# Kernel tuning notes

Hardware: AMD Instinct MI355X
Metric: run time of the kernel (lower is better)

Reference implementation:

```python
import jax, jax.numpy as jnp
import numpy as np

N_NODES = 50000
N_EDGES = 800000
N_GRAPHS = 512
IN_C, HID, OUT_C = 128, 256, 16


def _mlp(h, w1, b1, w2, b2):
    # PyG-style 2-layer MLP: Linear -> ReLU -> Linear (plain last layer)
    return jax.nn.relu(h @ w1 + b1) @ w2 + b2


def setup_inputs() -> dict:
    key = jax.random.key(0)
    ks = jax.random.split(key, 16)
    x = jax.random.normal(ks[0], (N_NODES, IN_C), dtype=jnp.float32)
    edge_index = jax.random.randint(ks[1], (2, N_EDGES), 0, N_NODES, dtype=jnp.int64)
    batch = jnp.sort(jax.random.randint(ks[2], (N_NODES,), 0, N_GRAPHS, dtype=jnp.int64))

    def lin(k, fan_in, fan_out):
        s = 1.0 / np.sqrt(fan_in)
        return jax.random.uniform(k, (fan_in, fan_out), jnp.float32, -s, s)

    inp = {"x": x, "edge_index": edge_index, "batch": batch}
    dims = [(IN_C, HID), (HID, HID), (HID, HID)]
    ki = 3
    for li, (din, dh) in enumerate(dims):
        inp[f"c{li}_w1"] = lin(ks[ki], din, dh); ki += 1
        inp[f"c{li}_b1"] = jnp.zeros((dh,), jnp.float32)
        inp[f"c{li}_w2"] = lin(ks[ki], dh, dh); ki += 1
        inp[f"c{li}_b2"] = jnp.zeros((dh,), jnp.float32)
    inp["out_w1"] = lin(ks[ki], HID, HID); ki += 1
    inp["out_b1"] = jnp.zeros((HID,), jnp.float32)
    inp["out_w2"] = lin(ks[ki], HID, OUT_C); ki += 1
    inp["out_b2"] = jnp.zeros((OUT_C,), jnp.float32)
    return inp


def reference(x, edge_index, batch,
              c0_w1, c0_b1, c0_w2, c0_b2,
              c1_w1, c1_b1, c1_w2, c1_b2,
              c2_w1, c2_b1, c2_w2, c2_b2,
              out_w1, out_b1, out_w2, out_b2):
    src, dst = edge_index[0], edge_index[1]
    params = [(c0_w1, c0_b1, c0_w2, c0_b2),
              (c1_w1, c1_b1, c1_w2, c1_b2),
              (c2_w1, c2_b1, c2_w2, c2_b2)]
    h = x
    for (w1, b1, w2, b2) in params:
        # GINConv with eps=0: MLP(x + sum_{j in N(i)} x_j)
        agg = jax.ops.segment_sum(h[src], dst, num_segments=N_NODES)
        h = _mlp(h + agg, w1, b1, w2, b2)
        h = jax.nn.relu(h)
        # dropout: identity (eval mode)
    # global mean pool over graphs
    sums = jax.ops.segment_sum(h, batch, num_segments=N_GRAPHS)
    counts = jax.ops.segment_sum(jnp.ones((N_NODES,), h.dtype), batch, num_segments=N_GRAPHS)
    pooled = sums / jnp.maximum(counts, 1.0)[:, None]
    return _mlp(pooled, out_w1, out_b1, out_w2, out_b2)
```

## Files before the change

### kernel.cpp

```cpp
#include <hip/hip_runtime.h>

#define N_NODES 50000
#define N_EDGES 800000
#define N_GRAPHS 512
#define IN_C 128
#define HID 256
#define OUT_C 16

typedef __attribute__((ext_vector_type(8))) short short8;
typedef __attribute__((ext_vector_type(4))) float f32x4;

__device__ __forceinline__ float bf2f(unsigned short u) {
    return __uint_as_float(((unsigned int)u) << 16);
}
__device__ __forceinline__ unsigned short f2bf(float f) {
    unsigned int u = __float_as_uint(f);
    u += 0x7fff + ((u >> 16) & 1);
    return (unsigned short)(u >> 16);
}

#define PLANE_ELEMS ((long)N_NODES * 32)

struct PrepArgs {
    const float* x;
    const float* w[6];
    ushort* xbf;
    ushort* wt[6];
    int* deg;
    float* sums;
};

__global__ __launch_bounds__(256) void prep_kernel(PrepArgs a) {
    const int X4    = N_NODES * IN_C / 4;
    const int TW    = IN_C * HID;
    const int TH    = HID * HID;
    const int TBASE = X4;
    const int TEND  = TBASE + TW + 5 * TH;
    const int D4    = N_NODES / 4;
    const int DBASE = TEND;
    const int SBASE = DBASE + D4;
    const int S4    = N_GRAPHS * HID / 4;
    const long total = (long)SBASE + S4;

    long stride = (long)gridDim.x * blockDim.x;
    for (long i = (long)blockIdx.x * blockDim.x + threadIdx.x; i < total; i += stride) {
        if (i < X4) {
            float4 v = ((const float4*)a.x)[i];
            ushort4 o;
            o.x = f2bf(v.x); o.y = f2bf(v.y); o.z = f2bf(v.z); o.w = f2bf(v.w);
            long e = i * 4;
            int node = (int)(e >> 7);
            int col  = (int)(e & 127);
            long off = (long)(col >> 5) * PLANE_ELEMS + (long)node * 32 + (col & 31);
            *(ushort4*)(a.xbf + off) = o;
        } else if (i < TEND) {
            long r = i - TBASE;
            int wi, shift;
            long off;
            if (r < TW) { wi = 0; shift = 7; off = r; }
            else { r -= TW; wi = 1 + (int)(r / TH); shift = 8; off = r % TH; }
            int n = (int)(off >> shift);
            int k = (int)(off - ((long)n << shift));
            a.wt[wi][off] = f2bf(a.w[wi][(long)k * HID + n]);
        } else if (i < SBASE) {
            ((int4*)a.deg)[i - DBASE] = make_int4(0, 0, 0, 0);
        } else {
            ((float4*)a.sums)[i - SBASE] = make_float4(0.f, 0.f, 0.f, 0.f);
        }
    }
}

__global__ void deg_kernel(const int* __restrict__ dst, int* __restrict__ deg) {
    int e = blockIdx.x * blockDim.x + threadIdx.x;
    if (e < N_EDGES) atomicAdd(&deg[dst[e]], 1);
}

__global__ __launch_bounds__(256) void scan_block(const int* __restrict__ deg,
                                                  int* __restrict__ partial,
                                                  int* __restrict__ blockSums) {
    __shared__ int s[256];
    int t = threadIdx.x;
    int i = blockIdx.x * 256 + t;
    int v = (i < N_NODES) ? deg[i] : 0;
    s[t] = v;
    __syncthreads();
    #pragma unroll
    for (int off = 1; off < 256; off <<= 1) {
        int add = (t >= off) ? s[t - off] : 0;
        __syncthreads();
        s[t] += add;
        __syncthreads();
    }
    if (i < N_NODES) partial[i] = s[t] - v;
    if (t == 255) blockSums[blockIdx.x] = s[255];
}

__global__ __launch_bounds__(256) void add_offsets_fused(
    const int* __restrict__ partial, const int* __restrict__ blockSums,
    int* __restrict__ rowptr, int* __restrict__ cursor, int nb) {
    __shared__ int s[256];
    __shared__ int myOff;
    int t = threadIdx.x;
    int v = (t < nb) ? blockSums[t] : 0;
    s[t] = v;
    __syncthreads();
    #pragma unroll
    for (int off = 1; off < 256; off <<= 1) {
        int add = (t >= off) ? s[t - off] : 0;
        __syncthreads();
        s[t] += add;
        __syncthreads();
    }
    if (t == blockIdx.x) myOff = s[t] - v;
    __syncthreads();
    int i = blockIdx.x * 256 + t;
    if (i < N_NODES) {
        int r = partial[i] + myOff;
        rowptr[i] = r;
        cursor[i] = r;
    }
    if (i == 0) rowptr[N_NODES] = N_EDGES;
}

__global__ void bucket_edges(const int* __restrict__ src, const int* __restrict__ dst,
                             int* __restrict__ cursor, int* __restrict__ srcSorted) {
    int e = blockIdx.x * blockDim.x + threadIdx.x;
    if (e >= N_EDGES) return;
    int p = atomicAdd(&cursor[dst[e]], 1);
    srcSorted[p] = src[e];
}

template <int C>
__global__ __launch_bounds__(256) void gin_aggregate_planar(
    const ushort* __restrict__ hp,
    const int* __restrict__ rowptr,
    const int* __restrict__ srcIdx,
    ushort* __restrict__ out)
{
    constexpr int NC  = C / 32;
    constexpr int PER = 8 / NC;

    int b  = blockIdx.x;
    int x8 = b & 7;
    int chunk   = x8 / PER;
    int nodeblk = (b >> 3) * PER + (x8 & (PER - 1));

    int lane = threadIdx.x & 63;
    int wave = threadIdx.x >> 6;
    int grp  = lane >> 2;
    int l    = lane & 3;
    int node = nodeblk * 64 + wave * 16 + grp;
    if (node >= N_NODES) return;

    const ushort* plane = hp + (long)chunk * PLANE_ELEMS + l * 8;

    float acc[8];
    {
        short8 sv = *(const short8*)(plane + (long)node * 32);
        #pragma unroll
        for (int v = 0; v < 8; ++v) acc[v] = bf2f((unsigned short)sv[v]);
    }

    int beg = rowptr[node], end = rowptr[node + 1];
    int k = beg;
    for (; k + 4 <= end; k += 4) {
        int si[4];
        #pragma unroll
        for (int u = 0; u < 4; ++u) si[u] = srcIdx[k + u];
        short8 r[4];
        #pragma unroll
        for (int u = 0; u < 4; ++u) r[u] = *(const short8*)(plane + (long)si[u] * 32);
        #pragma unroll
        for (int u = 0; u < 4; ++u)
            #pragma unroll
            for (int v = 0; v < 8; ++v) acc[v] += bf2f((unsigned short)r[u][v]);
    }
    for (; k < end; ++k) {
        short8 r = *(const short8*)(plane + (long)srcIdx[k] * 32);
        #pragma unroll
        for (int v = 0; v < 8; ++v) acc[v] += bf2f((unsigned short)r[v]);
    }

    short8 o;
    #pragma unroll
    for (int v = 0; v < 8; ++v) o[v] = (short)f2bf(acc[v]);
    *(short8*)(out + (long)node * C + chunk * 32 + l * 8) = o;
}

template <int K1, bool FUSE_POOL>
__global__ __launch_bounds__(512, 4) void gin_mlp(
    const ushort* __restrict__ A,
    const ushort* __restrict__ w1t,
    const float* __restrict__ b1,
    const ushort* __restrict__ w2t,
    const float* __restrict__ b2,
    ushort* __restrict__ out,
    const int* __restrict__ batch,
    float* __restrict__ sums,
    int M)
{
    __shared__ short Ls[2048 * 8];

    constexpr int NCH1 = K1 / 8;
    constexpr int NSLOT1 = 64 * NCH1;
    constexpr int NS1 = K1 / 32;

    int t = threadIdx.x;
    int lane = t & 63;
    int wv = t >> 6;
    int quad = lane >> 4;
    int l15 = lane & 15;
    int swz = l15 & 7;
    int row0 = blockIdx.x * 64;
    int col0 = wv * 32;

    short8 bw[16];
    #pragma unroll
    for (int s = 0; s < NS1; ++s)
        #pragma unroll
        for (int j = 0; j < 2; ++j)
            bw[s * 2 + j] = *(const short8*)(w1t + (long)(col0 + j * 16 + l15) * K1 + s * 32 + quad * 8);

    float bv[2];
    #pragma unroll
    for (int j = 0; j < 2; ++j) bv[j] = b1[col0 + j * 16 + l15];

    #pragma unroll
    for (int c = 0; c < NSLOT1; c += 512) {
        int s = c + t;
        int row = s / NCH1;
        int kcs = s & (NCH1 - 1);
        int kc = kcs ^ (row & 7);
        int grow = row0 + row;
        if (grow >= M) grow = M - 1;
        short8 v = *(const short8*)(A + (long)grow * K1 + kc * 8);
        *(short8*)&Ls[s * 8] = v;
    }
    __syncthreads();

    const f32x4 zero = {0.f, 0.f, 0.f, 0.f};
    f32x4 acc[4][2];
    #pragma unroll
    for (int i = 0; i < 4; ++i)
        #pragma unroll
        for (int j = 0; j < 2; ++j) acc[i][j] = zero;

    #pragma unroll
    for (int s = 0; s < NS1; ++s) {
        #pragma unroll
        for (int i = 0; i < 4; ++i) {
            int row = i * 16 + l15;
            int slot = row * NCH1 + ((s * 4 + quad) ^ swz);
            short8 a = *(const short8*)&Ls[slot * 8];
            acc[i][0] = __builtin_amdgcn_mfma_f32_16x16x32_bf16(a, bw[s * 2 + 0], acc[i][0], 0, 0, 0);
            acc[i][1] = __builtin_amdgcn_mfma_f32_16x16x32_bf16(a, bw[s * 2 + 1], acc[i][1], 0, 0, 0);
        }
    }

    #pragma unroll
    for (int s = 0; s < 8; ++s)
        #pragma unroll
        for (int j = 0; j < 2; ++j)
            bw[s * 2 + j] = *(const short8*)(w2t + (long)(col0 + j * 16 + l15) * 256 + s * 32 + quad * 8);

    __syncthreads();

    #pragma unroll
    for (int i = 0; i < 4; ++i)
        #pragma unroll
        for (int j = 0; j < 2; ++j) {
            int col = col0 + j * 16 + l15;
            int kc2 = col >> 3, sub = col & 7;
            #pragma unroll
            for (int r = 0; r < 4; ++r) {
                int row = i * 16 + quad * 4 + r;
                int slot = row * 32 + (kc2 ^ (row & 7));
                float o = fmaxf(acc[i][j][r] + bv[j], 0.f);
                Ls[slot * 8 + sub] = (short)f2bf(o);
            }
        }

    #pragma unroll
    for (int j = 0; j < 2; ++j) bv[j] = b2[col0 + j * 16 + l15];

    __syncthreads();

    #pragma unroll
    for (int i = 0; i < 4; ++i)
        #pragma unroll
        for (int j = 0; j < 2; ++j) acc[i][j] = zero;

    #pragma unroll
    for (int s = 0; s < 8; ++s) {
        #pragma unroll
        for (int i = 0; i < 4; ++i) {
            int row = i * 16 + l15;
            int slot = row * 32 + ((s * 4 + quad) ^ swz);
            short8 a = *(const short8*)&Ls[slot * 8];
            acc[i][0] = __builtin_amdgcn_mfma_f32_16x16x32_bf16(a, bw[s * 2 + 0], acc[i][0], 0, 0, 0);
            acc[i][1] = __builtin_amdgcn_mfma_f32_16x16x32_bf16(a, bw[s * 2 + 1], acc[i][1], 0, 0, 0);
        }
    }

    if constexpr (!FUSE_POOL) {
        #pragma unroll
        for (int i = 0; i < 4; ++i)
            #pragma unroll
            for (int r = 0; r < 4; ++r) {
                int row = row0 + i * 16 + quad * 4 + r;
                if (row >= M) continue;
                #pragma unroll
                for (int j = 0; j < 2; ++j) {
                    int col = col0 + j * 16 + l15;
                    float o = fmaxf(acc[i][j][r] + bv[j], 0.f);
                    out[(long)(col >> 5) * PLANE_ELEMS + (long)row * 32 + (col & 31)] = f2bf(o);
                }
            }
    } else {
        float pacc[2];
        #pragma unroll
        for (int j = 0; j < 2; ++j) pacc[j] = 0.f;
        int cur = -1;
        #pragma unroll
        for (int i = 0; i < 4; ++i) {
            #pragma unroll
            for (int r = 0; r < 4; ++r) {
                int row = row0 + i * 16 + quad * 4 + r;
                if (row >= M) continue;
                int g = batch[row];
                if (g != cur) {
                    if (cur >= 0) {
                        #pragma unroll
                        for (int j = 0; j < 2; ++j)
                            atomicAdd(&sums[(long)cur * 256 + col0 + j * 16 + l15], pacc[j]);
                    }
                    cur = g;
                    #pragma unroll
                    for (int j = 0; j < 2; ++j) pacc[j] = 0.f;
                }
                #pragma unroll
                for (int j = 0; j < 2; ++j)
                    pacc[j] += fmaxf(acc[i][j][r] + bv[j], 0.f);
            }
        }
        if (cur >= 0) {
            #pragma unroll
            for (int j = 0; j < 2; ++j)
                atomicAdd(&sums[(long)cur * 256 + col0 + j * 16 + l15], pacc[j]);
        }
    }
}

__global__ __launch_bounds__(256) void final_mlp_kernel(
    const float* __restrict__ sums, const int* __restrict__ batch,
    const float* __restrict__ w1, const float* __restrict__ b1,
    const float* __restrict__ w2, const float* __restrict__ b2,
    float* __restrict__ out) {
    __shared__ float row[HID];
    __shared__ float hid[HID];
    __shared__ int cntS;
    int g = blockIdx.x;
    int t = threadIdx.x;
    if (t == 0) {
        int lo = 0, hi = N_NODES;
        while (lo < hi) { int m = (lo + hi) >> 1; if (batch[m] < g) lo = m + 1; else hi = m; }
        int lo2 = lo, hi2 = N_NODES;
        while (lo2 < hi2) { int m = (lo2 + hi2) >> 1; if (batch[m] < g + 1) lo2 = m + 1; else hi2 = m; }
        cntS = lo2 - lo;
    }
    __syncthreads();
    float cnt = fmaxf((float)cntS, 1.0f);
    row[t] = sums[(long)g * HID + t] / cnt;
    __syncthreads();
    float acc = b1[t];
    for (int k = 0; k < HID; ++k) acc += row[k] * w1[k * HID + t];
    hid[t] = fmaxf(acc, 0.f);
    __syncthreads();
    if (t < OUT_C) {
        float o = b2[t];
        for (int k = 0; k < HID; ++k) o += hid[k] * w2[k * OUT_C + t];
        out[(long)g * OUT_C + t] = o;
    }
}

extern "C" void kernel_launch(void* const* d_in, const int* in_sizes, int n_in,
                              void* d_out, int out_size, void* d_ws, size_t ws_size,
                              hipStream_t stream) {
    const float* x     = (const float*)d_in[0];
    const int*   ei    = (const int*)d_in[1];
    const int*   batch = (const int*)d_in[2];
    const int*   src   = ei;
    const int*   dst   = ei + N_EDGES;

    const float* c_w1[3] = { (const float*)d_in[3],  (const float*)d_in[7],  (const float*)d_in[11] };
    const float* c_b1[3] = { (const float*)d_in[4],  (const float*)d_in[8],  (const float*)d_in[12] };
    const float* c_w2[3] = { (const float*)d_in[5],  (const float*)d_in[9],  (const float*)d_in[13] };
    const float* c_b2[3] = { (const float*)d_in[6],  (const float*)d_in[10], (const float*)d_in[14] };
    const float* out_w1 = (const float*)d_in[15];
    const float* out_b1 = (const float*)d_in[16];
    const float* out_w2 = (const float*)d_in[17];
    const float* out_b2 = (const float*)d_in[18];

    char* p = (char*)d_ws;
    auto alloc = [&](size_t bytes) {
        char* r = p;
        p += (bytes + 15) & ~(size_t)15;
        return r;
    };
    ushort* xbf  = (ushort*)alloc((size_t)N_NODES * IN_C * 2);
    ushort* bufA = (ushort*)alloc((size_t)N_NODES * HID * 2);
    ushort* bufB = (ushort*)alloc((size_t)N_NODES * HID * 2);
    ushort* wt[6];
    wt[0] = (ushort*)alloc((size_t)IN_C * HID * 2);
    for (int i = 1; i < 6; ++i) wt[i] = (ushort*)alloc((size_t)HID * HID * 2);
    float* sums   = (float*)alloc((size_t)N_GRAPHS * HID * 4);
    int* deg       = (int*)alloc((size_t)N_NODES * 4);
    int* rowptr    = (int*)alloc((size_t)(N_NODES + 1) * 4);
    int* blockSums = (int*)alloc(256 * 4);
    int* cursor    = (int*)alloc((size_t)N_NODES * 4);
    int* srcSorted = (int*)alloc((size_t)N_EDGES * 4);

    const int nb = (N_NODES + 255) / 256;

    {
        PrepArgs a;
        a.x = x;
        a.w[0] = c_w1[0]; a.w[1] = c_w2[0];
        a.w[2] = c_w1[1]; a.w[3] = c_w2[1];
        a.w[4] = c_w1[2]; a.w[5] = c_w2[2];
        a.xbf = xbf;
        for (int i = 0; i < 6; ++i) a.wt[i] = wt[i];
        a.deg = deg;
        a.sums = sums;
        prep_kernel<<<2048, 256, 0, stream>>>(a);
    }

    deg_kernel<<<(N_EDGES + 255) / 256, 256, 0, stream>>>(dst, deg);
    scan_block<<<nb, 256, 0, stream>>>(deg, rowptr, blockSums);
    add_offsets_fused<<<nb, 256, 0, stream>>>(rowptr, blockSums, rowptr, cursor, nb);
    bucket_edges<<<(N_EDGES + 255) / 256, 256, 0, stream>>>(src, dst, cursor, srcSorted);

    const int nodeBlks = (N_NODES + 63) / 64;
    const int aggX128  = nodeBlks * (IN_C / 32);
    const int aggX256  = nodeBlks * (HID / 32);
    const int mlpGrid  = (N_NODES + 63) / 64;

    gin_aggregate_planar<IN_C><<<aggX128, 256, 0, stream>>>(xbf, rowptr, srcSorted, bufB);
    gin_mlp<IN_C, false><<<mlpGrid, 512, 0, stream>>>(bufB, wt[0], c_b1[0], wt[1], c_b2[0],
                                                      bufA, batch, sums, N_NODES);

    gin_aggregate_planar<HID><<<aggX256, 256, 0, stream>>>(bufA, rowptr, srcSorted, bufB);
    gin_mlp<HID, false><<<mlpGrid, 512, 0, stream>>>(bufB, wt[2], c_b1[1], wt[3], c_b2[1],
                                                     bufA, batch, sums, N_NODES);

    gin_aggregate_planar<HID><<<aggX256, 256, 0, stream>>>(bufA, rowptr, srcSorted, bufB);
    gin_mlp<HID, true><<<mlpGrid, 512, 0, stream>>>(bufB, wt[4], c_b1[2], wt[5], c_b2[2],
                                                    bufA, batch, sums, N_NODES);

    final_mlp_kernel<<<N_GRAPHS, 256, 0, stream>>>(sums, batch, out_w1, out_b1,
                                                   out_w2, out_b2, (float*)d_out);
}
```

Measured before the change: 452.8 us.

## Sort nodes by degree for aggregation load balance and deepen gather unroll

Builds a degree histogram inside the scan kernel, scans it in descending order, and scatters nodes into a degree-sorted permutation that the aggregation kernel uses to choose which node each thread group handles. This puts nodes of similar degree in the same wavefront, cutting divergence from uneven neighbor counts. The gather loop is also unrolled to 8 edges with a 2-edge tail to keep more loads in flight. The cost is two extra small kernels, an extra indirection per node, and scattered output writes and self-row reads, since consecutive threads no longer handle consecutive nodes.

```diff
diff --git a/kernel.cpp b/kernel.cpp
--- a/kernel.cpp
+++ b/kernel.cpp
@@ -36,7 +36,7 @@
     const int TH    = HID * HID;
     const int TBASE = X4;
     const int TEND  = TBASE + TW + 5 * TH;
-    const int D4    = N_NODES / 4;
+    const int D4    = N_NODES / 4 + 64;
     const int DBASE = TEND;
     const int SBASE = DBASE + D4;
     const int S4    = N_GRAPHS * HID / 4;
@@ -77,13 +77,17 @@
 
 __global__ __launch_bounds__(256) void scan_block(const int* __restrict__ deg,
                                                   int* __restrict__ partial,
-                                                  int* __restrict__ blockSums) {
+                                                  int* __restrict__ blockSums,
+                                                  int* __restrict__ hist) {
     __shared__ int s[256];
+    __shared__ int hb[256];
     int t = threadIdx.x;
     int i = blockIdx.x * 256 + t;
     int v = (i < N_NODES) ? deg[i] : 0;
+    hb[t] = 0;
     s[t] = v;
     __syncthreads();
+    if (i < N_NODES) atomicAdd(&hb[v < 255 ? v : 255], 1);
     #pragma unroll
     for (int off = 1; off < 256; off <<= 1) {
         int add = (t >= off) ? s[t - off] : 0;
@@ -93,6 +97,8 @@
     }
     if (i < N_NODES) partial[i] = s[t] - v;
     if (t == 255) blockSums[blockIdx.x] = s[255];
+    __syncthreads();
+    if (hb[t]) atomicAdd(&hist[t], hb[t]);
 }
 
 __global__ __launch_bounds__(256) void add_offsets_fused(
@@ -130,11 +136,38 @@
     srcSorted[p] = src[e];
 }
 
+__global__ __launch_bounds__(256) void hist_scan(const int* __restrict__ hist,
+                                                 int* __restrict__ binCursor) {
+    __shared__ int s[256];
+    int t = threadIdx.x;
+    int v = hist[255 - t];
+    s[t] = v;
+    __syncthreads();
+    #pragma unroll
+    for (int off = 1; off < 256; off <<= 1) {
+        int add = (t >= off) ? s[t - off] : 0;
+        __syncthreads();
+        s[t] += add;
+        __syncthreads();
+    }
+    binCursor[255 - t] = s[t] - v;
+}
+
+__global__ void perm_scatter(const int* __restrict__ deg, int* __restrict__ binCursor,
+                             int* __restrict__ perm) {
+    int i = blockIdx.x * blockDim.x + threadIdx.x;
+    if (i >= N_NODES) return;
+    int d = deg[i]; d = d < 255 ? d : 255;
+    int p = atomicAdd(&binCursor[d], 1);
+    perm[p] = i;
+}
+
 template <int C>
 __global__ __launch_bounds__(256) void gin_aggregate_planar(
     const ushort* __restrict__ hp,
     const int* __restrict__ rowptr,
     const int* __restrict__ srcIdx,
+    const int* __restrict__ perm,
     ushort* __restrict__ out)
 {
     constexpr int NC  = C / 32;
@@ -149,8 +182,9 @@
     int wave = threadIdx.x >> 6;
     int grp  = lane >> 2;
     int l    = lane & 3;
-    int node = nodeblk * 64 + wave * 16 + grp;
-    if (node >= N_NODES) return;
+    int slot = nodeblk * 64 + wave * 16 + grp;
+    if (slot >= N_NODES) return;
+    int node = perm[slot];
 
     const ushort* plane = hp + (long)chunk * PLANE_ELEMS + l * 8;
 
@@ -163,19 +197,28 @@
 
     int beg = rowptr[node], end = rowptr[node + 1];
     int k = beg;
-    for (; k + 4 <= end; k += 4) {
-        int si[4];
-        #pragma unroll
-        for (int u = 0; u < 4; ++u) si[u] = srcIdx[k + u];
-        short8 r[4];
-        #pragma unroll
-        for (int u = 0; u < 4; ++u) r[u] = *(const short8*)(plane + (long)si[u] * 32);
-        #pragma unroll
-        for (int u = 0; u < 4; ++u)
+    for (; k + 8 <= end; k += 8) {
+        int si[8];
+        #pragma unroll
+        for (int u = 0; u < 8; ++u) si[u] = srcIdx[k + u];
+        short8 r[8];
+        #pragma unroll
+        for (int u = 0; u < 8; ++u) r[u] = *(const short8*)(plane + (long)si[u] * 32);
+        #pragma unroll
+        for (int u = 0; u < 8; ++u)
             #pragma unroll
             for (int v = 0; v < 8; ++v) acc[v] += bf2f((unsigned short)r[u][v]);
     }
-    for (; k < end; ++k) {
+    for (; k + 2 <= end; k += 2) {
+        int si0 = srcIdx[k], si1 = srcIdx[k + 1];
+        short8 r0 = *(const short8*)(plane + (long)si0 * 32);
+        short8 r1 = *(const short8*)(plane + (long)si1 * 32);
+        #pragma unroll
+        for (int v = 0; v < 8; ++v) acc[v] += bf2f((unsigned short)r0[v]);
+        #pragma unroll
+        for (int v = 0; v < 8; ++v) acc[v] += bf2f((unsigned short)r1[v]);
+    }
+    if (k < end) {
         short8 r = *(const short8*)(plane + (long)srcIdx[k] * 32);
         #pragma unroll
         for (int v = 0; v < 8; ++v) acc[v] += bf2f((unsigned short)r[v]);
@@ -415,9 +458,12 @@
     for (int i = 1; i < 6; ++i) wt[i] = (ushort*)alloc((size_t)HID * HID * 2);
     float* sums   = (float*)alloc((size_t)N_GRAPHS * HID * 4);
     int* deg       = (int*)alloc((size_t)N_NODES * 4);
+    int* hist      = (int*)alloc(256 * 4);
     int* rowptr    = (int*)alloc((size_t)(N_NODES + 1) * 4);
     int* blockSums = (int*)alloc(256 * 4);
     int* cursor    = (int*)alloc((size_t)N_NODES * 4);
+    int* binCursor = (int*)alloc(256 * 4);
+    int* perm      = (int*)alloc((size_t)N_NODES * 4);
     int* srcSorted = (int*)alloc((size_t)N_EDGES * 4);
 
     const int nb = (N_NODES + 255) / 256;
@@ -436,24 +482,26 @@
     }
 
     deg_kernel<<<(N_EDGES + 255) / 256, 256, 0, stream>>>(dst, deg);
-    scan_block<<<nb, 256, 0, stream>>>(deg, rowptr, blockSums);
+    scan_block<<<nb, 256, 0, stream>>>(deg, rowptr, blockSums, hist);
     add_offsets_fused<<<nb, 256, 0, stream>>>(rowptr, blockSums, rowptr, cursor, nb);
     bucket_edges<<<(N_EDGES + 255) / 256, 256, 0, stream>>>(src, dst, cursor, srcSorted);
+    hist_scan<<<1, 256, 0, stream>>>(hist, binCursor);
+    perm_scatter<<<nb, 256, 0, stream>>>(deg, binCursor, perm);
 
     const int nodeBlks = (N_NODES + 63) / 64;
     const int aggX128  = nodeBlks * (IN_C / 32);
     const int aggX256  = nodeBlks * (HID / 32);
     const int mlpGrid  = (N_NODES + 63) / 64;
 
-    gin_aggregate_planar<IN_C><<<aggX128, 256, 0, stream>>>(xbf, rowptr, srcSorted, bufB);
+    gin_aggregate_planar<IN_C><<<aggX128, 256, 0, stream>>>(xbf, rowptr, srcSorted, perm, bufB);
     gin_mlp<IN_C, false><<<mlpGrid, 512, 0, stream>>>(bufB, wt[0], c_b1[0], wt[1], c_b2[0],
                                                       bufA, batch, sums, N_NODES);
 
-    gin_aggregate_planar<HID><<<aggX256, 256, 0, stream>>>(bufA, rowptr, srcSorted, bufB);
+    gin_aggregate_planar<HID><<<aggX256, 256, 0, stream>>>(bufA, rowptr, srcSorted, perm, bufB);
     gin_mlp<HID, false><<<mlpGrid, 512, 0, stream>>>(bufB, wt[2], c_b1[1], wt[3], c_b2[1],
                                                      bufA, batch, sums, N_NODES);
 
-    gin_aggregate_planar<HID><<<aggX256, 256, 0, stream>>>(bufA, rowptr, srcSorted, bufB);
+    gin_aggregate_planar<HID><<<aggX256, 256, 0, stream>>>(bufA, rowptr, srcSorted, perm, bufB);
     gin_mlp<HID, true><<<mlpGrid, 512, 0, stream>>>(bufB, wt[4], c_b1[2], wt[5], c_b2[2],
                                                     bufA, batch, sums, N_NODES);
 
```

After: 609.7 us. 1.35x slower.
